# Optimization experiments

Hardware: AMD Instinct MI355X
Metric: run time of the kernel (lower is better)

The kernel has to match this reference:

```python
import jax, jax.numpy as jnp
import numpy as np

B, N, D, H = 2, 2048, 1024, 16
HD = D // H


def precompute_freqs_cis(dim, end, theta=10000.0):
    freqs = 1.0 / theta ** (jnp.arange(0, dim, 2)[: dim // 2].astype(jnp.float32) / dim)
    t = jnp.arange(end, dtype=jnp.float32)
    freqs = jnp.outer(t, freqs)  # [N, dim//2]
    return jax.lax.complex(jnp.cos(freqs), jnp.sin(freqs))


def apply_rotary(q, k, freqs_cis):
    # q,k: [B,H,N,HD]; freqs_cis: [N, HD//2] broadcasts over B,H
    qr = q.reshape(q.shape[:-1] + (-1, 2))
    kr = k.reshape(k.shape[:-1] + (-1, 2))
    qc = jax.lax.complex(qr[..., 0], qr[..., 1]) * freqs_cis
    kc = jax.lax.complex(kr[..., 0], kr[..., 1]) * freqs_cis
    q_out = jnp.stack([jnp.real(qc), jnp.imag(qc)], axis=-1).reshape(q.shape)
    k_out = jnp.stack([jnp.real(kc), jnp.imag(kc)], axis=-1).reshape(k.shape)
    return q_out, k_out


def setup_inputs() -> dict:
    key = jax.random.key(0)
    ks = jax.random.split(key, 5)
    s = 1.0 / np.sqrt(D)
    return {
        "x": jax.random.normal(ks[0], (B, N, D), dtype=jnp.float32),
        "Wq": jax.random.normal(ks[1], (D, D), dtype=jnp.float32) * s,
        "Wk": jax.random.normal(ks[2], (D, D), dtype=jnp.float32) * s,
        "Wv": jax.random.normal(ks[3], (D, D), dtype=jnp.float32) * s,
        "Wo": jax.random.normal(ks[4], (D, D), dtype=jnp.float32) * s,
    }


def reference(x, Wq, Wk, Wv, Wo):
    b, n, d = x.shape
    h, hd = H, d // H
    q = (x @ Wq).reshape(b, n, h, hd).transpose(0, 2, 1, 3)
    k = (x @ Wk).reshape(b, n, h, hd).transpose(0, 2, 1, 3)
    v = (x @ Wv).reshape(b, n, h, hd).transpose(0, 2, 1, 3)
    freqs_cis = precompute_freqs_cis(hd, n)
    q, k = apply_rotary(q, k, freqs_cis)
    scale = hd ** (-0.5)
    attn = jnp.einsum("bhqd,bhkd->bhqk", q, k) * scale
    attn = jax.nn.softmax(attn, axis=-1)
    out = jnp.einsum("bhqk,bhkd->bhqd", attn, v)
    out = out.transpose(0, 2, 1, 3).reshape(b, n, d)
    return out @ Wo
```

## Files before the change

### kernel.cpp

```cpp
#include <hip/hip_runtime.h>

typedef unsigned short u16;
typedef short  bf16x8 __attribute__((ext_vector_type(8)));
typedef u16    u16x8  __attribute__((ext_vector_type(8)));
typedef float  f32x4  __attribute__((ext_vector_type(4)));
typedef float  f32x2  __attribute__((ext_vector_type(2)));
typedef int    i32x4  __attribute__((ext_vector_type(4)));
typedef unsigned u32x2 __attribute__((ext_vector_type(2)));
typedef unsigned u32x4 __attribute__((ext_vector_type(4)));

__device__ __forceinline__ u16 f2bf(float f) {
  union { float f; unsigned u; } x; x.f = f;
  return (u16)((x.u + 0x7fffu + ((x.u >> 16) & 1u)) >> 16);
}

__device__ __forceinline__ unsigned pk2bf(float a, float b) {
  unsigned r;
  asm("v_cvt_pk_bf16_f32 %0, %1, %2" : "=v"(r) : "v"(a), "v"(b));
  return r;
}

__device__ __forceinline__ float exp2v(float x) {
  float r;
  asm("v_exp_f32 %0, %1" : "=v"(r) : "v"(x));
  return r;
}

__device__ __forceinline__ void gload16(const void* g, void* lds) {
  __builtin_amdgcn_global_load_lds((const __attribute__((address_space(1))) unsigned int*)g,
                                   (__attribute__((address_space(3))) unsigned int*)lds,
                                   16, 0, 0);
}

__device__ __forceinline__ bf16x8 lds8(const u16* base, int row, int colb) {
  int off = (row << 7) + colb;
  off ^= (row & 7) << 4;
  return *(const bf16x8*)((const char*)base + off);
}

__device__ __forceinline__ bf16x8 vfrag(const u16* base, int row, int colb) {
  int off = (row << 7) + colb;
  off ^= (row & 7) << 4;
  const char* p = (const char*)base;
  u32x2 a = *(const u32x2*)(p + off);
  u32x2 b = *(const u32x2*)(p + (off ^ 32));
  u32x4 t; t[0] = a[0]; t[1] = a[1]; t[2] = b[0]; t[3] = b[1];
  return *(const bf16x8*)&t;
}

__device__ __forceinline__ bf16x8 lds32(const u16* base, int row, int lg) {
  int off = (row << 6) + ((lg ^ (row & 3)) << 4);
  return *(const bf16x8*)((const char*)base + off);
}


__global__ __launch_bounds__(256) void cast_x_k(const float* __restrict__ x,
                                                u16* __restrict__ xb) {
  int i = (blockIdx.x * 256 + threadIdx.x) * 8;
  float4 a = *(const float4*)&x[i];
  float4 b = *(const float4*)&x[i + 4];
  u16x8 o;
  o[0] = f2bf(a.x); o[1] = f2bf(a.y); o[2] = f2bf(a.z); o[3] = f2bf(a.w);
  o[4] = f2bf(b.x); o[5] = f2bf(b.y); o[6] = f2bf(b.z); o[7] = f2bf(b.w);
  *(u16x8*)&xb[i] = o;
}

__global__ __launch_bounds__(256) void transpose_cast_k(const float* __restrict__ Wq,
                                                        const float* __restrict__ Wk,
                                                        const float* __restrict__ Wv,
                                                        const float* __restrict__ Wo,
                                                        u16* __restrict__ WqkvT,
                                                        u16* __restrict__ WoT) {
  __shared__ u16 tile[64][72];
  int z = blockIdx.z;
  const float* W = (z == 0) ? Wq : (z == 1) ? Wk : (z == 2) ? Wv : Wo;
  u16* dst = (z < 3) ? (WqkvT + z * 1024 * 1024) : WoT;
  int k0 = blockIdx.y << 6, nn0 = blockIdx.x << 6;
  int t = threadIdx.x;
#pragma unroll
  for (int p = 0; p < 4; ++p) {
    int kr = (p << 4) + (t >> 4), c4 = (t & 15) << 2;
    float4 v = *(const float4*)&W[(k0 + kr) * 1024 + nn0 + c4];
    tile[c4 + 0][kr] = f2bf(v.x); tile[c4 + 1][kr] = f2bf(v.y);
    tile[c4 + 2][kr] = f2bf(v.z); tile[c4 + 3][kr] = f2bf(v.w);
  }
  __syncthreads();
#pragma unroll
  for (int p = 0; p < 2; ++p) {
    int nr = (p << 5) + (t >> 3), c8 = (t & 7) << 3;
    i32x4 vv = *(const i32x4*)&tile[nr][c8];
    *(i32x4*)&dst[(nn0 + nr) * 1024 + k0 + c8] = vv;
  }
}

__global__ __launch_bounds__(256) void rope_table_k(f32x2* __restrict__ ctab) {
  int idx = blockIdx.x * 256 + threadIdx.x;
  int i = idx & 31, p = idx >> 5;
  float freq = powf(10000.0f, -(float)(2 * i) * (1.0f / 64.0f));
  float ang = (float)p * freq;
  f32x2 v; v[0] = cosf(ang); v[1] = sinf(ang);
  ctab[idx] = v;
}


__global__ __launch_bounds__(256) void gemm_qkv_k(const u16* __restrict__ A,
                                                  const u16* __restrict__ BT,
                                                  u16* __restrict__ Qb,
                                                  u16* __restrict__ Kb,
                                                  u16* __restrict__ VbT,
                                                  const f32x2* __restrict__ ctab) {
  __shared__ u16 As[3][128 * 32];
  __shared__ u16 Bs[3][128 * 32];
  const int K = 1024;
  const int m0 = blockIdx.y << 7, n0 = blockIdx.x << 7;
  const int t = threadIdx.x, w = t >> 6, l = t & 63;
  const int wr = (w >> 1) << 6, wc = (w & 1) << 6;
  const int lr = l & 15, lg = l >> 4;
  const int g_row = l >> 2;
  const int g_col = (((l & 3) ^ ((l >> 2) & 3)) << 3);

#define QKV_STAGE(buf, kt)                                                            \
  {                                                                                   \
    const int k0_ = (kt) << 5;                                                        \
    _Pragma("unroll") for (int it = 0; it < 2; ++it) {                                \
      int seg = (w << 1) + it;                                                        \
      int row = (seg << 4) + g_row;                                                   \
      gload16(&A[(m0 + row) * K + k0_ + g_col], (char*)As[buf] + seg * 1024);         \
      gload16(&BT[(n0 + row) * K + k0_ + g_col], (char*)Bs[buf] + seg * 1024);        \
    }                                                                                 \
  }

  f32x4 acc[4][4] = {};

  QKV_STAGE(0, 0)
  QKV_STAGE(1, 1)

#pragma unroll
  for (int kt = 0; kt < 32; ++kt) {
    if (kt < 31) asm volatile("s_waitcnt vmcnt(4)" ::: "memory");
    else         asm volatile("s_waitcnt vmcnt(0)" ::: "memory");
    __builtin_amdgcn_s_barrier();
    __builtin_amdgcn_sched_barrier(0);
    if (kt < 30) { QKV_STAGE((kt + 2) % 3, kt + 2) }
    const u16* Ab = As[kt % 3];
    const u16* Bb = Bs[kt % 3];
    bf16x8 af[4], bfr[4];
#pragma unroll
    for (int m = 0; m < 4; ++m) af[m] = lds32(Ab, wr + (m << 4) + lr, lg);
#pragma unroll
    for (int n = 0; n < 4; ++n) bfr[n] = lds32(Bb, wc + (n << 4) + lr, lg);
#pragma unroll
    for (int m = 0; m < 4; ++m)
#pragma unroll
      for (int n = 0; n < 4; ++n)
        acc[m][n] = __builtin_amdgcn_mfma_f32_16x16x32_bf16(af[m], bfr[n], acc[m][n], 0, 0, 0);
  }
#undef QKV_STAGE

  const int region = n0 >> 10;
  if (region < 2) {
    const float qscale = 0.125f * 1.44269504088896f;
#pragma unroll
    for (int m = 0; m < 4; ++m)
#pragma unroll
      for (int n = 0; n < 4; ++n) {
        const int col = n0 + wc + (n << 4) + lr;
        const int hd = col & 63;
#pragma unroll
        for (int r = 0; r < 4; ++r) {
          const int row = m0 + wr + (m << 4) + (lg << 2) + r;
          float v = acc[m][n][r];
          float p = __shfl_xor(v, 1);
          f32x2 cs = ctab[(row & 2047) * 32 + (hd >> 1)];
          float o = (hd & 1) ? (p * cs[1] + v * cs[0]) : (v * cs[0] - p * cs[1]);
          if (region == 0) { o *= qscale; Qb[row * 1024 + (col & 1023)] = f2bf(o); }
          else             { Kb[row * 1024 + (col & 1023)] = f2bf(o); }
        }
      }
  } else {
#pragma unroll
    for (int m = 0; m < 4; ++m)
#pragma unroll
      for (int n = 0; n < 4; ++n) {
        const int cv = n0 + wc + (n << 4) + lr - 2048;
        const int hh = cv >> 6, dim = cv & 63;
#pragma unroll
        for (int r = 0; r < 4; ++r) {
          const int row = m0 + wr + (m << 4) + (lg << 2) + r;
          const int bb = row >> 11, pos = row & 2047;
          VbT[(((bb << 4) + hh) << 6 | dim) * 2048 + pos] = f2bf(acc[m][n][r]);
        }
      }
  }
}


__global__ __launch_bounds__(256) void gemm_out_k(const u16* __restrict__ A,
                                                  const u16* __restrict__ BT,
                                                  float* __restrict__ C) {
  __shared__ u16 As[3][64 * 32];
  __shared__ u16 Bs[3][128 * 32];
  const int K = 1024;
  const int m0 = blockIdx.y << 6, n0 = blockIdx.x << 7;
  const int t = threadIdx.x, w = t >> 6, l = t & 63;
  const int wr = (w & 1) << 5, wc = (w >> 1) << 6;
  const int lr = l & 15, lg = l >> 4;
  const int g_row = l >> 2;
  const int g_col = (((l & 3) ^ ((l >> 2) & 3)) << 3);

#define OUT_STAGE(buf, kt)                                                            \
  {                                                                                   \
    const int k0_ = (kt) << 5;                                                        \
    {                                                                                 \
      int rowA = (w << 4) + g_row;                                                    \
      gload16(&A[(m0 + rowA) * K + k0_ + g_col], (char*)As[buf] + w * 1024);          \
    }                                                                                 \
    _Pragma("unroll") for (int it = 0; it < 2; ++it) {                                \
      int seg = (w << 1) + it;                                                        \
      int row = (seg << 4) + g_row;                                                   \
      gload16(&BT[(n0 + row) * K + k0_ + g_col], (char*)Bs[buf] + seg * 1024);        \
    }                                                                                 \
  }

  f32x4 acc[2][4] = {};

  OUT_STAGE(0, 0)
  OUT_STAGE(1, 1)

#pragma unroll
  for (int kt = 0; kt < 32; ++kt) {
    if (kt < 31) asm volatile("s_waitcnt vmcnt(3)" ::: "memory");
    else         asm volatile("s_waitcnt vmcnt(0)" ::: "memory");
    __builtin_amdgcn_s_barrier();
    __builtin_amdgcn_sched_barrier(0);
    if (kt < 30) { OUT_STAGE((kt + 2) % 3, kt + 2) }
    const u16* Ab = As[kt % 3];
    const u16* Bb = Bs[kt % 3];
    bf16x8 af[2], bfr[4];
#pragma unroll
    for (int m = 0; m < 2; ++m) af[m] = lds32(Ab, wr + (m << 4) + lr, lg);
#pragma unroll
    for (int n = 0; n < 4; ++n) bfr[n] = lds32(Bb, wc + (n << 4) + lr, lg);
#pragma unroll
    for (int m = 0; m < 2; ++m)
#pragma unroll
      for (int n = 0; n < 4; ++n)
        acc[m][n] = __builtin_amdgcn_mfma_f32_16x16x32_bf16(af[m], bfr[n], acc[m][n], 0, 0, 0);
  }
#undef OUT_STAGE

#pragma unroll
  for (int m = 0; m < 2; ++m)
#pragma unroll
    for (int n = 0; n < 4; ++n) {
      const int col = n0 + wc + (n << 4) + lr;
#pragma unroll
      for (int r = 0; r < 4; ++r) {
        const int row = m0 + wr + (m << 4) + (lg << 2) + r;
        C[row * 1024 + col] = acc[m][n][r];
      }
    }
}


#define SOFTMAX_C0 (-12.0f)

__global__ __launch_bounds__(256) void attn_k(const u16* __restrict__ Qb,
                                              const u16* __restrict__ Kb,
                                              const u16* __restrict__ VbT,
                                              u16* __restrict__ Ob) {
  __shared__ u16 Qs[128 * 64];
  __shared__ u16 Ks[3][64 * 64];
  __shared__ u16 Vs[3][64 * 64];

  const int lin = blockIdx.y * 16 + blockIdx.x;
  const int xcd = lin & 7, rest = lin >> 3;
  const int bh = (xcd << 2) + (rest & 3);
  const int qt = rest >> 2;
  const int b = bh >> 4;
  const int t = threadIdx.x, w = t >> 6, l = t & 63;
  const int lr = l & 15, lg = l >> 4;
  const int rb = b << 11;
  const int cb = (bh & 15) << 6;
  const int srow = l >> 3;
  const int scol = ((l & 7) ^ srow) << 3;

#define KV_STAGE(buf, tile)                                                                        \
  {                                                                                                \
    _Pragma("unroll") for (int it = 0; it < 2; ++it) {                                             \
      int seg = (w << 1) + it;                                                                     \
      int row = (seg << 3) + srow;                                                                 \
      gload16(&Kb[(rb + ((tile) << 6) + row) * 1024 + cb + scol], (char*)Ks[buf] + seg * 1024);    \
      gload16(&VbT[((bh << 6) + row) * 2048 + ((tile) << 6) + scol], (char*)Vs[buf] + seg * 1024); \
    }                                                                                              \
  }

#pragma unroll
  for (int it = 0; it < 4; ++it) {
    int seg = (w << 2) + it;
    int row = (seg << 3) + srow;
    gload16(&Qb[(rb + (qt << 7) + row) * 1024 + cb + scol], (char*)Qs + seg * 1024);
  }
  KV_STAGE(0, 0)
  KV_STAGE(1, 1)

  asm volatile("s_waitcnt vmcnt(8)" ::: "memory");
  __builtin_amdgcn_s_barrier();
  __builtin_amdgcn_sched_barrier(0);

  bf16x8 qf[2][2];
#pragma unroll
  for (int g = 0; g < 2; ++g)
#pragma unroll
    for (int kk = 0; kk < 2; ++kk)
      qf[g][kk] = lds8(Qs, (w << 5) + (g << 4) + lr, (kk << 6) + (lg << 4));

  float lsum[2] = {0.f, 0.f};
  f32x4 Oacc[2][4] = {};

  int cur = 0;
  for (int kt = 0; kt < 32; ++kt) {
    if (kt < 31) asm volatile("s_waitcnt vmcnt(4)" ::: "memory");
    else         asm volatile("s_waitcnt vmcnt(0)" ::: "memory");
    __builtin_amdgcn_s_barrier();
    __builtin_amdgcn_sched_barrier(0);

    if (kt < 30) {
      const int nb = (cur == 0) ? 2 : cur - 1;
      KV_STAGE(nb, kt + 2)
    }

    f32x4 S[2][4];
#pragma unroll
    for (int g = 0; g < 2; ++g)
#pragma unroll
      for (int c = 0; c < 4; ++c) S[g][c] = (f32x4){SOFTMAX_C0, SOFTMAX_C0, SOFTMAX_C0, SOFTMAX_C0};
#pragma unroll
    for (int kk = 0; kk < 2; ++kk) {
      bf16x8 kf[4];
#pragma unroll
      for (int c = 0; c < 4; ++c) kf[c] = lds8(Ks[cur], (c << 4) + lr, (kk << 6) + (lg << 4));
      __builtin_amdgcn_s_setprio(1);
#pragma unroll
      for (int c = 0; c < 4; ++c) {
        S[0][c] = __builtin_amdgcn_mfma_f32_16x16x32_bf16(kf[c], qf[0][kk], S[0][c], 0, 0, 0);
        S[1][c] = __builtin_amdgcn_mfma_f32_16x16x32_bf16(kf[c], qf[1][kk], S[1][c], 0, 0, 0);
      }
      __builtin_amdgcn_s_setprio(0);
    }

    unsigned U[2][4][2];
#pragma unroll
    for (int g = 0; g < 2; ++g)
#pragma unroll
      for (int c = 0; c < 4; ++c) {
        float p0 = exp2v(S[g][c][0]), p1 = exp2v(S[g][c][1]);
        float p2 = exp2v(S[g][c][2]), p3 = exp2v(S[g][c][3]);
        lsum[g] += (p0 + p1) + (p2 + p3);
        U[g][c][0] = pk2bf(p0, p1);
        U[g][c][1] = pk2bf(p2, p3);
      }

#pragma unroll
    for (int kk2 = 0; kk2 < 2; ++kk2) {
      bf16x8 vf[4];
#pragma unroll
      for (int df = 0; df < 4; ++df)
        vf[df] = vfrag(Vs[cur], (df << 4) + lr, (kk2 << 6) + (lg << 3));
      __builtin_amdgcn_s_setprio(1);
#pragma unroll
      for (int g = 0; g < 2; ++g) {
        u32x4 pt;
        pt[0] = U[g][2 * kk2][0];     pt[1] = U[g][2 * kk2][1];
        pt[2] = U[g][2 * kk2 + 1][0]; pt[3] = U[g][2 * kk2 + 1][1];
        bf16x8 pa = *(const bf16x8*)&pt;
#pragma unroll
        for (int df = 0; df < 4; ++df)
          Oacc[g][df] = __builtin_amdgcn_mfma_f32_16x16x32_bf16(pa, vf[df], Oacc[g][df], 0, 0, 0);
      }
      __builtin_amdgcn_s_setprio(0);
    }

    cur = (cur == 2) ? 0 : cur + 1;
  }
#undef KV_STAGE

#pragma unroll
  for (int g = 0; g < 2; ++g) {
    float ls = lsum[g];
    ls += __shfl_xor(ls, 16);
    ls += __shfl_xor(ls, 32);
    float lq[4];
#pragma unroll
    for (int r = 0; r < 4; ++r) lq[r] = 1.f / __shfl(ls, (lg << 2) + r);
#pragma unroll
    for (int df = 0; df < 4; ++df)
#pragma unroll
      for (int r = 0; r < 4; ++r) {
        int row = (qt << 7) + (w << 5) + (g << 4) + (lg << 2) + r;
        int col = (df << 4) + lr;
        Ob[(rb + row) * 1024 + cb + col] = f2bf(Oacc[g][df][r] * lq[r]);
      }
  }
}


extern "C" void kernel_launch(void* const* d_in, const int* in_sizes, int n_in,
                              void* d_out, int out_size, void* d_ws, size_t ws_size,
                              hipStream_t stream) {
  const float* x  = (const float*)d_in[0];
  const float* Wq = (const float*)d_in[1];
  const float* Wk = (const float*)d_in[2];
  const float* Wv = (const float*)d_in[3];
  const float* Wo = (const float*)d_in[4];
  float* out = (float*)d_out;

  char* ws = (char*)d_ws;
  u16* xb     = (u16*)(ws);
  u16* WqkvT  = (u16*)(ws + 8388608);
  u16* WoT    = (u16*)(ws + 14680064);
  u16* Qb     = (u16*)(ws + 16777216);
  u16* Kb     = (u16*)(ws + 25165824);
  u16* VbT    = (u16*)(ws + 33554432);
  f32x2* ctab = (f32x2*)(ws + 41943040);
  u16* Ob = xb;

  cast_x_k<<<2048, 256, 0, stream>>>(x, xb);
  dim3 gt(16, 16, 4);
  transpose_cast_k<<<gt, 256, 0, stream>>>(Wq, Wk, Wv, Wo, WqkvT, WoT);
  rope_table_k<<<256, 256, 0, stream>>>(ctab);

  dim3 gq(24, 32);
  gemm_qkv_k<<<gq, 256, 0, stream>>>(xb, WqkvT, Qb, Kb, VbT, ctab);

  dim3 ga(16, 32);
  attn_k<<<ga, 256, 0, stream>>>(Qb, Kb, VbT, Ob);

  dim3 go(8, 64);
  gemm_out_k<<<go, 256, 0, stream>>>(Ob, WoT, out);
}
```

Baseline: 122.7 us.

## Restructure attention into two-wave blocks with register Q and permuted V layout

The attention kernel now uses 128-thread blocks in which each wave owns 64 query rows. Q fragments are loaded straight from global memory into registers instead of being staged through LDS, and K/V staging drops from triple to double buffering. The QKV GEMM writes V^T with a permuted position order so each V fragment becomes a single 16-byte LDS read instead of two 8-byte reads. The constant softmax offset is also removed. Together these aim to cut LDS traffic and instructions per tile, at the cost of fewer waves per block, more registers per wave, a shallower prefetch pipeline, and exp2 of the raw scores without the offset.

```diff
diff --git a/kernel.cpp b/kernel.cpp
--- a/kernel.cpp
+++ b/kernel.cpp
@@ -6,7 +6,6 @@
 typedef float  f32x4  __attribute__((ext_vector_type(4)));
 typedef float  f32x2  __attribute__((ext_vector_type(2)));
 typedef int    i32x4  __attribute__((ext_vector_type(4)));
-typedef unsigned u32x2 __attribute__((ext_vector_type(2)));
 typedef unsigned u32x4 __attribute__((ext_vector_type(4)));
 
 __device__ __forceinline__ u16 f2bf(float f) {
@@ -36,16 +35,6 @@
   int off = (row << 7) + colb;
   off ^= (row & 7) << 4;
   return *(const bf16x8*)((const char*)base + off);
-}
-
-__device__ __forceinline__ bf16x8 vfrag(const u16* base, int row, int colb) {
-  int off = (row << 7) + colb;
-  off ^= (row & 7) << 4;
-  const char* p = (const char*)base;
-  u32x2 a = *(const u32x2*)(p + off);
-  u32x2 b = *(const u32x2*)(p + (off ^ 32));
-  u32x4 t; t[0] = a[0]; t[1] = a[1]; t[2] = b[0]; t[3] = b[1];
-  return *(const bf16x8*)&t;
 }
 
 __device__ __forceinline__ bf16x8 lds32(const u16* base, int row, int lg) {
@@ -188,7 +177,11 @@
         for (int r = 0; r < 4; ++r) {
           const int row = m0 + wr + (m << 4) + (lg << 2) + r;
           const int bb = row >> 11, pos = row & 2047;
-          VbT[(((bb << 4) + hh) << 6 | dim) * 2048 + pos] = f2bf(acc[m][n][r]);
+          const int k6 = pos & 63;
+          const int pp = (k6 & 3) | (((k6 >> 4) & 1) << 2) | (((k6 >> 2) & 3) << 3)
+                       | (((k6 >> 5) & 1) << 5);
+          const int posp = (pos & ~63) | pp;
+          VbT[(((bb << 4) + hh) << 6 | dim) * 2048 + posp] = f2bf(acc[m][n][r]);
         }
       }
   }
@@ -263,17 +256,14 @@
 }
 
 
-#define SOFTMAX_C0 (-12.0f)
-
-__global__ __launch_bounds__(256) void attn_k(const u16* __restrict__ Qb,
+__global__ __launch_bounds__(128) void attn_k(const u16* __restrict__ Qb,
                                               const u16* __restrict__ Kb,
                                               const u16* __restrict__ VbT,
                                               u16* __restrict__ Ob) {
-  __shared__ u16 Qs[128 * 64];
-  __shared__ u16 Ks[3][64 * 64];
-  __shared__ u16 Vs[3][64 * 64];
-
-  const int lin = blockIdx.y * 16 + blockIdx.x;
+  __shared__ u16 Ks[2][64 * 64];
+  __shared__ u16 Vs[2][64 * 64];
+
+  const int lin = blockIdx.x;
   const int xcd = lin & 7, rest = lin >> 3;
   const int bh = (xcd << 2) + (rest & 3);
   const int qt = rest >> 2;
@@ -287,89 +277,71 @@
 
 #define KV_STAGE(buf, tile)                                                                        \
   {                                                                                                \
-    _Pragma("unroll") for (int it = 0; it < 2; ++it) {                                             \
-      int seg = (w << 1) + it;                                                                     \
+    _Pragma("unroll") for (int it = 0; it < 4; ++it) {                                             \
+      int seg = (w << 2) + it;                                                                     \
       int row = (seg << 3) + srow;                                                                 \
       gload16(&Kb[(rb + ((tile) << 6) + row) * 1024 + cb + scol], (char*)Ks[buf] + seg * 1024);    \
       gload16(&VbT[((bh << 6) + row) * 2048 + ((tile) << 6) + scol], (char*)Vs[buf] + seg * 1024); \
     }                                                                                              \
   }
 
-#pragma unroll
-  for (int it = 0; it < 4; ++it) {
-    int seg = (w << 2) + it;
-    int row = (seg << 3) + srow;
-    gload16(&Qb[(rb + (qt << 7) + row) * 1024 + cb + scol], (char*)Qs + seg * 1024);
-  }
+  bf16x8 qf[4][2];
+#pragma unroll
+  for (int g = 0; g < 4; ++g)
+#pragma unroll
+    for (int kk = 0; kk < 2; ++kk)
+      qf[g][kk] = *(const bf16x8*)&Qb[(rb + (qt << 7) + (w << 6) + (g << 4) + lr) * 1024
+                                      + cb + (kk << 5) + (lg << 3)];
+
   KV_STAGE(0, 0)
-  KV_STAGE(1, 1)
-
-  asm volatile("s_waitcnt vmcnt(8)" ::: "memory");
-  __builtin_amdgcn_s_barrier();
-  __builtin_amdgcn_sched_barrier(0);
-
-  bf16x8 qf[2][2];
-#pragma unroll
-  for (int g = 0; g < 2; ++g)
-#pragma unroll
-    for (int kk = 0; kk < 2; ++kk)
-      qf[g][kk] = lds8(Qs, (w << 5) + (g << 4) + lr, (kk << 6) + (lg << 4));
-
-  float lsum[2] = {0.f, 0.f};
-  f32x4 Oacc[2][4] = {};
+
+  const f32x4 z4 = {0.f, 0.f, 0.f, 0.f};
+  float lsum[4] = {0.f, 0.f, 0.f, 0.f};
+  f32x4 Oacc[4][4] = {};
 
   int cur = 0;
   for (int kt = 0; kt < 32; ++kt) {
-    if (kt < 31) asm volatile("s_waitcnt vmcnt(4)" ::: "memory");
+    __builtin_amdgcn_s_barrier();
+    if (kt < 31) { KV_STAGE(cur ^ 1, kt + 1) }
+    if (kt < 31) asm volatile("s_waitcnt vmcnt(8)" ::: "memory");
     else         asm volatile("s_waitcnt vmcnt(0)" ::: "memory");
-    __builtin_amdgcn_s_barrier();
     __builtin_amdgcn_sched_barrier(0);
 
-    if (kt < 30) {
-      const int nb = (cur == 0) ? 2 : cur - 1;
-      KV_STAGE(nb, kt + 2)
-    }
-
-    f32x4 S[2][4];
-#pragma unroll
-    for (int g = 0; g < 2; ++g)
-#pragma unroll
-      for (int c = 0; c < 4; ++c) S[g][c] = (f32x4){SOFTMAX_C0, SOFTMAX_C0, SOFTMAX_C0, SOFTMAX_C0};
-#pragma unroll
-    for (int kk = 0; kk < 2; ++kk) {
-      bf16x8 kf[4];
-#pragma unroll
-      for (int c = 0; c < 4; ++c) kf[c] = lds8(Ks[cur], (c << 4) + lr, (kk << 6) + (lg << 4));
+    const u16* Kc = Ks[cur];
+    const u16* Vc = Vs[cur];
+
+    unsigned U[4][4][2];
+#pragma unroll
+    for (int c = 0; c < 4; ++c) {
+      bf16x8 kf0 = lds8(Kc, (c << 4) + lr, (lg << 4));
+      bf16x8 kf1 = lds8(Kc, (c << 4) + lr, 64 + (lg << 4));
+      f32x4 S[4];
       __builtin_amdgcn_s_setprio(1);
 #pragma unroll
-      for (int c = 0; c < 4; ++c) {
-        S[0][c] = __builtin_amdgcn_mfma_f32_16x16x32_bf16(kf[c], qf[0][kk], S[0][c], 0, 0, 0);
-        S[1][c] = __builtin_amdgcn_mfma_f32_16x16x32_bf16(kf[c], qf[1][kk], S[1][c], 0, 0, 0);
+      for (int g = 0; g < 4; ++g) {
+        S[g] = __builtin_amdgcn_mfma_f32_16x16x32_bf16(kf0, qf[g][0], z4, 0, 0, 0);
+        S[g] = __builtin_amdgcn_mfma_f32_16x16x32_bf16(kf1, qf[g][1], S[g], 0, 0, 0);
       }
       __builtin_amdgcn_s_setprio(0);
-    }
-
-    unsigned U[2][4][2];
-#pragma unroll
-    for (int g = 0; g < 2; ++g)
-#pragma unroll
-      for (int c = 0; c < 4; ++c) {
-        float p0 = exp2v(S[g][c][0]), p1 = exp2v(S[g][c][1]);
-        float p2 = exp2v(S[g][c][2]), p3 = exp2v(S[g][c][3]);
+#pragma unroll
+      for (int g = 0; g < 4; ++g) {
+        float p0 = exp2v(S[g][0]), p1 = exp2v(S[g][1]);
+        float p2 = exp2v(S[g][2]), p3 = exp2v(S[g][3]);
         lsum[g] += (p0 + p1) + (p2 + p3);
         U[g][c][0] = pk2bf(p0, p1);
         U[g][c][1] = pk2bf(p2, p3);
       }
+    }
 
 #pragma unroll
     for (int kk2 = 0; kk2 < 2; ++kk2) {
       bf16x8 vf[4];
 #pragma unroll
       for (int df = 0; df < 4; ++df)
-        vf[df] = vfrag(Vs[cur], (df << 4) + lr, (kk2 << 6) + (lg << 3));
+        vf[df] = lds8(Vc, (df << 4) + lr, (kk2 << 6) + (lg << 4));
       __builtin_amdgcn_s_setprio(1);
 #pragma unroll
-      for (int g = 0; g < 2; ++g) {
+      for (int g = 0; g < 4; ++g) {
         u32x4 pt;
         pt[0] = U[g][2 * kk2][0];     pt[1] = U[g][2 * kk2][1];
         pt[2] = U[g][2 * kk2 + 1][0]; pt[3] = U[g][2 * kk2 + 1][1];
@@ -381,12 +353,12 @@
       __builtin_amdgcn_s_setprio(0);
     }
 
-    cur = (cur == 2) ? 0 : cur + 1;
+    cur ^= 1;
   }
 #undef KV_STAGE
 
 #pragma unroll
-  for (int g = 0; g < 2; ++g) {
+  for (int g = 0; g < 4; ++g) {
     float ls = lsum[g];
     ls += __shfl_xor(ls, 16);
     ls += __shfl_xor(ls, 32);
@@ -397,7 +369,7 @@
     for (int df = 0; df < 4; ++df)
 #pragma unroll
       for (int r = 0; r < 4; ++r) {
-        int row = (qt << 7) + (w << 5) + (g << 4) + (lg << 2) + r;
+        int row = (qt << 7) + (w << 6) + (g << 4) + (lg << 2) + r;
         int col = (df << 4) + lr;
         Ob[(rb + row) * 1024 + cb + col] = f2bf(Oacc[g][df][r] * lq[r]);
       }
@@ -433,8 +405,7 @@
   dim3 gq(24, 32);
   gemm_qkv_k<<<gq, 256, 0, stream>>>(xb, WqkvT, Qb, Kb, VbT, ctab);
 
-  dim3 ga(16, 32);
-  attn_k<<<ga, 256, 0, stream>>>(Qb, Kb, VbT, Ob);
+  attn_k<<<512, 128, 0, stream>>>(Qb, Kb, VbT, Ob);
 
   dim3 go(8, 64);
   gemm_out_k<<<go, 256, 0, stream>>>(Ob, WoT, out);
```

New measurement: 148.0 us. 1.21x slower.
